# Performance work log

Hardware: AMD Instinct MI355X
Metric: run time of the kernel (lower is better)

The kernel has to match this reference:

```python
import jax, jax.numpy as jnp
import numpy as np

ALPHA = 0.2      # LeakyReLU negative slope
DROPOUT_P = 0.1  # torch F.dropout default training=True, so it IS applied
D_OUT = 128


def setup_inputs() -> dict:
    key = jax.random.key(0)
    k1, k2, k3 = jax.random.split(key, 3)
    N, D_IN = 8192, 128
    batch = jax.random.normal(k1, (N, D_IN), dtype=jnp.float32)
    # xavier_uniform gain=1.414 scale for faithfulness of magnitude
    w = jax.random.uniform(k2, (D_IN, D_OUT), dtype=jnp.float32, minval=-1.0, maxval=1.0) * (1.414 * np.sqrt(6.0 / (D_IN + D_OUT)))
    a = jax.random.uniform(k3, (2 * D_OUT, 1), dtype=jnp.float32, minval=-1.0, maxval=1.0) * (1.414 * np.sqrt(6.0 / (2 * D_OUT + 1)))
    return {"batch": batch, "w": w, "a": a}


def reference(batch, w, a):
    h = batch.reshape(-1, w.shape[0])            # [N, D_in]
    Wh = h @ w                                   # [N, D_out]
    Wh1 = Wh @ a[:D_OUT, :]                      # [N, 1]
    Wh2 = Wh @ a[D_OUT:, :]                      # [N, 1]
    e = Wh1 + Wh2.T                              # [N, N] additive scores
    e = jnp.where(e > 0, e, ALPHA * e)           # LeakyReLU
    attention = jax.nn.softmax(e, axis=1)        # row softmax
    # dropout with a fixed key (deterministic reference)
    keep = jax.random.bernoulli(jax.random.key(42), 1.0 - DROPOUT_P, attention.shape)
    attention = jnp.where(keep, attention / (1.0 - DROPOUT_P), 0.0)
    h_prime = attention @ Wh                     # [N, D_out]
    return jax.nn.elu(h_prime)                   # concat=True -> elu
```

## Files before the change

### kernel.cpp

```cpp
#include <hip/hip_runtime.h>
#include <stdint.h>

#define ALPHA 0.2f
#define LOG2E 1.4426950408889634f

typedef __bf16 bf16x8 __attribute__((ext_vector_type(8)));
typedef float f32x4 __attribute__((ext_vector_type(4)));

__device__ __forceinline__ uint32_t rotl32(uint32_t x, int r) {
  return __builtin_amdgcn_alignbit(x, x, 32 - r);
}

__device__ __forceinline__ uint32_t tf_mix(uint32_t f) {
  const uint32_t ks1 = 42u, ks2 = 0x1BD11BF0u;
  uint32_t x0 = 0u;
  uint32_t x1 = f + ks1;
#define TFR(r) { x0 += x1; x1 = rotl32(x1, r); x1 ^= x0; }
  TFR(13) TFR(15) TFR(26) TFR(6)  x0 += ks1; x1 += ks2 + 1u;
  TFR(17) TFR(29) TFR(16) TFR(24) x0 += ks2; x1 += 0u  + 2u;
  TFR(13) TFR(15) TFR(26) TFR(6)  x0 += 0u;  x1 += ks1 + 3u;
  TFR(17) TFR(29) TFR(16) TFR(24) x0 += ks1; x1 += ks2 + 4u;
  TFR(13) TFR(15) TFR(26) TFR(6)  x0 += ks2; x1 += 0u  + 5u;
#undef TFR
  return x0 ^ x1;
}

__device__ __forceinline__ void tf_mix4(uint32_t f0, uint32_t f1, uint32_t f2, uint32_t f3,
                                        uint32_t& o0, uint32_t& o1, uint32_t& o2, uint32_t& o3) {
  const uint32_t ks1 = 42u, ks2 = 0x1BD11BF0u;
  uint32_t a0 = 0u, a1 = 0u, a2 = 0u, a3 = 0u;
  uint32_t b0 = f0 + ks1, b1 = f1 + ks1, b2 = f2 + ks1, b3 = f3 + ks1;
#define Q4(rr)                                                              \
  a0 += b0; a1 += b1; a2 += b2; a3 += b3;                                   \
  b0 = rotl32(b0, rr); b1 = rotl32(b1, rr);                                 \
  b2 = rotl32(b2, rr); b3 = rotl32(b3, rr);                                 \
  b0 ^= a0; b1 ^= a1; b2 ^= a2; b3 ^= a3;
#define KADD(c0, c1)                                                        \
  a0 += (c0); a1 += (c0); a2 += (c0); a3 += (c0);                           \
  b0 += (c1); b1 += (c1); b2 += (c1); b3 += (c1);
  Q4(13) Q4(15) Q4(26) Q4(6)  KADD(ks1, ks2 + 1u)
  Q4(17) Q4(29) Q4(16) Q4(24) KADD(ks2, 0u + 2u)
  Q4(13) Q4(15) Q4(26) Q4(6)  KADD(0u, ks1 + 3u)
  Q4(17) Q4(29) Q4(16) Q4(24) KADD(ks1, ks2 + 4u)
  Q4(13) Q4(15) Q4(26) Q4(6)  KADD(ks2, 0u + 5u)
#undef Q4
#undef KADD
  o0 = a0 ^ b0; o1 = a1 ^ b1; o2 = a2 ^ b2; o3 = a3 ^ b3;
}

__device__ __forceinline__ unsigned short f2bf(float f) {
  uint32_t u = __float_as_uint(f);
  return (unsigned short)((u + 0x7fffu + ((u >> 16) & 1u)) >> 16);
}

__global__ __launch_bounds__(256) void wh_kernel(
    const float* __restrict__ batch, const float* __restrict__ w,
    const float* __restrict__ a, unsigned short* __restrict__ whb2,
    float* __restrict__ s1, float* __restrict__ s2, uint32_t* __restrict__ s2key) {
  __shared__ float whlds[32][128];
  int t = threadIdx.x;
  int i0 = blockIdx.x * 32;
  int d = t & 127, rg = t >> 7;
  int ib = i0 + rg * 16;
  float acc[16];
#pragma unroll
  for (int r = 0; r < 16; ++r) acc[r] = 0.f;
  for (int k = 0; k < 128; k += 4) {
    float wv0 = w[(k + 0) * 128 + d];
    float wv1 = w[(k + 1) * 128 + d];
    float wv2 = w[(k + 2) * 128 + d];
    float wv3 = w[(k + 3) * 128 + d];
#pragma unroll
    for (int r = 0; r < 16; ++r) {
      float4 b4 = *(const float4*)&batch[(ib + r) * 128 + k];
      acc[r] = fmaf(b4.w, wv3, fmaf(b4.z, wv2, fmaf(b4.y, wv1, fmaf(b4.x, wv0, acc[r]))));
    }
  }
  unsigned short hb[16];
#pragma unroll
  for (int r = 0; r < 16; ++r) {
    whlds[rg * 16 + r][d] = acc[r];
    hb[r] = f2bf(acc[r]);
  }
  uint32_t pk[8];
#pragma unroll
  for (int q = 0; q < 8; ++q) pk[q] = (uint32_t)hb[2 * q] | ((uint32_t)hb[2 * q + 1] << 16);
  uint32_t base0 = (((uint32_t)(ib >> 3) * 16u + (uint32_t)(d & 15)) * 8u + (uint32_t)(d >> 4)) * 8u;
  *(uint4*)&whb2[base0]        = make_uint4(pk[0], pk[1], pk[2], pk[3]);
  *(uint4*)&whb2[base0 + 1024] = make_uint4(pk[4], pk[5], pk[6], pk[7]);
  __syncthreads();
  int rr = t >> 3, seg = t & 7, c0 = seg * 16;
  const float* wr = &whlds[rr][c0];
  float p1 = 0.f, p2 = 0.f;
#pragma unroll
  for (int c = 0; c < 16; ++c) {
    float v = wr[c];
    p1 = fmaf(v, a[c0 + c], p1);
    p2 = fmaf(v, a[128 + c0 + c], p2);
  }
  p1 += __shfl_xor(p1, 1, 64); p1 += __shfl_xor(p1, 2, 64); p1 += __shfl_xor(p1, 4, 64);
  p2 += __shfl_xor(p2, 1, 64); p2 += __shfl_xor(p2, 2, 64); p2 += __shfl_xor(p2, 4, 64);
  if (seg == 0) { s1[i0 + rr] = p1; s2[i0 + rr] = p2; }
  float v = (seg == 0) ? p2 : -3.4e38f;
#pragma unroll
  for (int m = 1; m <= 32; m <<= 1) v = fmaxf(v, __shfl_xor(v, m, 64));
  if ((t & 63) == 0) {
    uint32_t b = __float_as_uint(v);
    uint32_t key = (b & 0x80000000u) ? ~b : (b | 0x80000000u);
    atomicMax(s2key, key);
  }
}

__global__ __launch_bounds__(256, 4) void gat_main(
    const float* __restrict__ s1, const float* __restrict__ s2g,
    const uint32_t* __restrict__ s2key, const unsigned short* __restrict__ whb2,
    float* __restrict__ pacc, float* __restrict__ pz) {
  __shared__ __align__(16) float smem[4160];
  int t = threadIdx.x;
  int rb = blockIdx.x >> 2, ck = blockIdx.x & 3;
  int R0 = rb * 16, C0 = ck * 2048;

  for (int k = t; k < 512; k += 256) {
    float4 v4 = ((const float4*)(s2g + C0))[k];
    float sL, e1, e2;
    sL = v4.x * LOG2E; e1 = __builtin_amdgcn_exp2f(sL); e2 = __builtin_amdgcn_exp2f(ALPHA * sL);
    ((float2*)smem)[k * 4 + 0] = make_float2(e1, e2);
    sL = v4.y * LOG2E; e1 = __builtin_amdgcn_exp2f(sL); e2 = __builtin_amdgcn_exp2f(ALPHA * sL);
    ((float2*)smem)[k * 4 + 1] = make_float2(e1, e2);
    sL = v4.z * LOG2E; e1 = __builtin_amdgcn_exp2f(sL); e2 = __builtin_amdgcn_exp2f(ALPHA * sL);
    ((float2*)smem)[k * 4 + 2] = make_float2(e1, e2);
    sL = v4.w * LOG2E; e1 = __builtin_amdgcn_exp2f(sL); e2 = __builtin_amdgcn_exp2f(ALPHA * sL);
    ((float2*)smem)[k * 4 + 3] = make_float2(e1, e2);
  }

  uint32_t kk = *s2key;
  uint32_t mb = (kk & 0x80000000u) ? (kk ^ 0x80000000u) : ~kk;
  float s2maxL = __uint_as_float(mb) * LOG2E;

  int w = t >> 6, lane = t & 63;
  int r = lane & 15, q = lane >> 4;

  float s1L = s1[R0 + r] * LOG2E;
  float xmL = s1L + s2maxL;
  float mrL = fmaxf(xmL, ALPHA * xmL);
  float F1 = __builtin_amdgcn_exp2f(s1L - mrL);
  float F2 = __builtin_amdgcn_exp2f(fmaf(ALPHA, s1L, -mrL));

  uint32_t fcur = (uint32_t)(R0 + r) * 8192u + (uint32_t)(C0 + w * 32 + q * 8);
  uint32_t voff = (((uint32_t)(C0 / 8 + w * 4 + q)) * 16u + (uint32_t)r) * 128u;
  const char* pB = (const char*)whb2;
  const float2* Eb = ((const float2*)smem) + w * 32 + q * 8;

  f32x4 acc0 = {0,0,0,0}, acc1 = {0,0,0,0}, acc2 = {0,0,0,0}, acc3 = {0,0,0,0};
  f32x4 acc4 = {0,0,0,0}, acc5 = {0,0,0,0}, acc6 = {0,0,0,0}, acc7 = {0,0,0,0};
  float z0 = 0.f, z1 = 0.f;
  const uint32_t KTH = 0xE6666600u;

  __syncthreads();

#pragma unroll 1
  for (int it = 0; it < 16; ++it) {
    bf16x8 B0 = *(const bf16x8*)(pB + voff);
    bf16x8 B1 = *(const bf16x8*)(pB + voff + 16);
    bf16x8 B2 = *(const bf16x8*)(pB + voff + 32);
    bf16x8 B3 = *(const bf16x8*)(pB + voff + 48);
    bf16x8 B4 = *(const bf16x8*)(pB + voff + 64);
    bf16x8 B5 = *(const bf16x8*)(pB + voff + 80);
    bf16x8 B6 = *(const bf16x8*)(pB + voff + 96);
    bf16x8 B7 = *(const bf16x8*)(pB + voff + 112);
    float4 E01 = *(const float4*)(Eb);
    float4 E23 = *(const float4*)(Eb + 2);
    float4 E45 = *(const float4*)(Eb + 4);
    float4 E67 = *(const float4*)(Eb + 6);
    __builtin_amdgcn_sched_barrier(0);

    bf16x8 A;
    {
      uint32_t h0, h1, h2, h3;
      tf_mix4(fcur + 0u, fcur + 1u, fcur + 2u, fcur + 3u, h0, h1, h2, h3);
      float pv0 = fmaxf(F1 * E01.x, F2 * E01.y);
      float pv1 = fmaxf(F1 * E01.z, F2 * E01.w);
      float pv2 = fmaxf(F1 * E23.x, F2 * E23.y);
      float pv3 = fmaxf(F1 * E23.z, F2 * E23.w);
      z0 += pv0 + pv1;
      z1 += pv2 + pv3;
      A[0] = (__bf16)((h0 < KTH) ? pv0 : 0.f);
      A[1] = (__bf16)((h1 < KTH) ? pv1 : 0.f);
      A[2] = (__bf16)((h2 < KTH) ? pv2 : 0.f);
      A[3] = (__bf16)((h3 < KTH) ? pv3 : 0.f);
    }
    {
      uint32_t h4, h5, h6, h7;
      tf_mix4(fcur + 4u, fcur + 5u, fcur + 6u, fcur + 7u, h4, h5, h6, h7);
      float pv4 = fmaxf(F1 * E45.x, F2 * E45.y);
      float pv5 = fmaxf(F1 * E45.z, F2 * E45.w);
      float pv6 = fmaxf(F1 * E67.x, F2 * E67.y);
      float pv7 = fmaxf(F1 * E67.z, F2 * E67.w);
      z0 += pv4 + pv5;
      z1 += pv6 + pv7;
      A[4] = (__bf16)((h4 < KTH) ? pv4 : 0.f);
      A[5] = (__bf16)((h5 < KTH) ? pv5 : 0.f);
      A[6] = (__bf16)((h6 < KTH) ? pv6 : 0.f);
      A[7] = (__bf16)((h7 < KTH) ? pv7 : 0.f);
    }

    acc0 = __builtin_amdgcn_mfma_f32_16x16x32_bf16(A, B0, acc0, 0, 0, 0);
    acc1 = __builtin_amdgcn_mfma_f32_16x16x32_bf16(A, B1, acc1, 0, 0, 0);
    acc2 = __builtin_amdgcn_mfma_f32_16x16x32_bf16(A, B2, acc2, 0, 0, 0);
    acc3 = __builtin_amdgcn_mfma_f32_16x16x32_bf16(A, B3, acc3, 0, 0, 0);
    acc4 = __builtin_amdgcn_mfma_f32_16x16x32_bf16(A, B4, acc4, 0, 0, 0);
    acc5 = __builtin_amdgcn_mfma_f32_16x16x32_bf16(A, B5, acc5, 0, 0, 0);
    acc6 = __builtin_amdgcn_mfma_f32_16x16x32_bf16(A, B6, acc6, 0, 0, 0);
    acc7 = __builtin_amdgcn_mfma_f32_16x16x32_bf16(A, B7, acc7, 0, 0, 0);

    fcur += 128u;
    voff += 32768u;
    Eb += 128;
  }
  float z = z0 + z1;

  __syncthreads();
  float zq = z + __shfl_xor(z, 16, 64);
  zq += __shfl_xor(zq, 32, 64);
  if (lane < 16) smem[4096 + w * 16 + lane] = zq;

  float* red = smem;
  int wbase = w * 1024 + q * 256 + r;
#define STOREG(u, accN)                                \
  {                                                    \
    red[wbase + 0 * 64 + (u) * 16] = accN[0];          \
    red[wbase + 1 * 64 + (u) * 16] = accN[1];          \
    red[wbase + 2 * 64 + (u) * 16] = accN[2];          \
    red[wbase + 3 * 64 + (u) * 16] = accN[3];          \
  }
  STOREG(0, acc0) STOREG(1, acc1) STOREG(2, acc2) STOREG(3, acc3)
  __syncthreads();
#pragma unroll
  for (int k2 = 0; k2 < 4; ++k2) {
    int idx = t * 4 + k2;
    float s = (red[idx] + red[1024 + idx]) + (red[2048 + idx] + red[3072 + idx]);
    atomicAdd(&pacc[(R0 + (idx >> 6)) * 128 + (idx & 63)], s);
  }
  __syncthreads();
  STOREG(0, acc4) STOREG(1, acc5) STOREG(2, acc6) STOREG(3, acc7)
#undef STOREG
  __syncthreads();
#pragma unroll
  for (int k2 = 0; k2 < 4; ++k2) {
    int idx = t * 4 + k2;
    float s = (red[idx] + red[1024 + idx]) + (red[2048 + idx] + red[3072 + idx]);
    atomicAdd(&pacc[(R0 + (idx >> 6)) * 128 + 64 + (idx & 63)], s);
  }
  if (t < 16) {
    float zs = (smem[4096 + t] + smem[4112 + t]) + (smem[4128 + t] + smem[4144 + t]);
    atomicAdd(&pz[R0 + t], zs);
  }
}

__global__ __launch_bounds__(256) void gat_final(
    const float* __restrict__ pacc, const float* __restrict__ pz,
    float* __restrict__ out) {
  int t = threadIdx.x;
  int row = blockIdx.x * 8 + (t >> 5);
  int d4 = (t & 31) * 4;
  float zinv = 1.f / (0.9f * pz[row]);
  float4 p = *(const float4*)&pacc[row * 128 + d4];
  float4 o;
  float v;
  v = p.x * zinv; o.x = v > 0.f ? v : expm1f(v);
  v = p.y * zinv; o.y = v > 0.f ? v : expm1f(v);
  v = p.z * zinv; o.z = v > 0.f ? v : expm1f(v);
  v = p.w * zinv; o.w = v > 0.f ? v : expm1f(v);
  *(float4*)&out[row * 128 + d4] = o;
}

extern "C" void kernel_launch(void* const* d_in, const int* in_sizes, int n_in,
                              void* d_out, int out_size, void* d_ws, size_t ws_size,
                              hipStream_t stream) {
  const float* batch = (const float*)d_in[0];
  const float* w = (const float*)d_in[1];
  const float* a = (const float*)d_in[2];
  float* out = (float*)d_out;
  char* ws = (char*)d_ws;
  float* pacc = (float*)ws;
  float* pz = (float*)(ws + 4194304);
  uint32_t* s2key = (uint32_t*)(ws + 4194304 + 32768);
  unsigned short* whb2 = (unsigned short*)(ws + 4194304 + 32768 + 64);
  float* s1 = (float*)(ws + 4194304 + 32768 + 64 + 2097152);
  float* s2 = (float*)(ws + 4194304 + 32768 + 64 + 2097152 + 32768);

  hipMemsetAsync(ws, 0, 4194304 + 32768 + 64, stream);
  wh_kernel<<<256, 256, 0, stream>>>(batch, w, a, whb2, s1, s2, s2key);
  gat_main<<<2048, 256, 0, stream>>>(s1, s2, s2key, whb2, pacc, pz);
  gat_final<<<1024, 256, 0, stream>>>(pacc, pz, out);
}
```

Measured before the change: 176.5 us.

## Compute exp per element in-loop, split columns in two, and replace atomics with slabs

The main kernel no longer precomputes two exponentials per column in shared memory. It stores log2-scaled s2 and evaluates exp2 of the LeakyReLU score per element, which halves the LDS reads per iteration. Each block now covers 4096 columns instead of 2048, so there are half as many blocks. Each block writes its partial accumulators and row sums to a per-split slab instead of using global atomics, and the final kernel adds the two slabs. The large workspace memset shrinks to the 64-byte key. The trade is more transcendental work per element and fewer blocks with a longer loop. The B loads are also split into two halves around the first half of the compute.

Measured after the change: 211.1 us. 19.6% more time.

```diff
diff --git a/kernel.cpp b/kernel.cpp
--- a/kernel.cpp
+++ b/kernel.cpp
@@ -9,20 +9,6 @@
 
 __device__ __forceinline__ uint32_t rotl32(uint32_t x, int r) {
   return __builtin_amdgcn_alignbit(x, x, 32 - r);
-}
-
-__device__ __forceinline__ uint32_t tf_mix(uint32_t f) {
-  const uint32_t ks1 = 42u, ks2 = 0x1BD11BF0u;
-  uint32_t x0 = 0u;
-  uint32_t x1 = f + ks1;
-#define TFR(r) { x0 += x1; x1 = rotl32(x1, r); x1 ^= x0; }
-  TFR(13) TFR(15) TFR(26) TFR(6)  x0 += ks1; x1 += ks2 + 1u;
-  TFR(17) TFR(29) TFR(16) TFR(24) x0 += ks2; x1 += 0u  + 2u;
-  TFR(13) TFR(15) TFR(26) TFR(6)  x0 += 0u;  x1 += ks1 + 3u;
-  TFR(17) TFR(29) TFR(16) TFR(24) x0 += ks1; x1 += ks2 + 4u;
-  TFR(13) TFR(15) TFR(26) TFR(6)  x0 += ks2; x1 += 0u  + 5u;
-#undef TFR
-  return x0 ^ x1;
 }
 
 __device__ __forceinline__ void tf_mix4(uint32_t f0, uint32_t f1, uint32_t f2, uint32_t f3,
@@ -114,23 +100,18 @@
 __global__ __launch_bounds__(256, 4) void gat_main(
     const float* __restrict__ s1, const float* __restrict__ s2g,
     const uint32_t* __restrict__ s2key, const unsigned short* __restrict__ whb2,
-    float* __restrict__ pacc, float* __restrict__ pz) {
+    float* __restrict__ pslab, float* __restrict__ zslab) {
   __shared__ __align__(16) float smem[4160];
   int t = threadIdx.x;
-  int rb = blockIdx.x >> 2, ck = blockIdx.x & 3;
-  int R0 = rb * 16, C0 = ck * 2048;
-
-  for (int k = t; k < 512; k += 256) {
+  int rb = blockIdx.x >> 1, ck = blockIdx.x & 1;
+  int R0 = rb * 16, C0 = ck * 4096;
+  float* ps = pslab + ck * (8192 * 128);
+  float* zs = zslab + ck * 8192;
+
+  for (int k = t; k < 1024; k += 256) {
     float4 v4 = ((const float4*)(s2g + C0))[k];
-    float sL, e1, e2;
-    sL = v4.x * LOG2E; e1 = __builtin_amdgcn_exp2f(sL); e2 = __builtin_amdgcn_exp2f(ALPHA * sL);
-    ((float2*)smem)[k * 4 + 0] = make_float2(e1, e2);
-    sL = v4.y * LOG2E; e1 = __builtin_amdgcn_exp2f(sL); e2 = __builtin_amdgcn_exp2f(ALPHA * sL);
-    ((float2*)smem)[k * 4 + 1] = make_float2(e1, e2);
-    sL = v4.z * LOG2E; e1 = __builtin_amdgcn_exp2f(sL); e2 = __builtin_amdgcn_exp2f(ALPHA * sL);
-    ((float2*)smem)[k * 4 + 2] = make_float2(e1, e2);
-    sL = v4.w * LOG2E; e1 = __builtin_amdgcn_exp2f(sL); e2 = __builtin_amdgcn_exp2f(ALPHA * sL);
-    ((float2*)smem)[k * 4 + 3] = make_float2(e1, e2);
+    v4.x *= LOG2E; v4.y *= LOG2E; v4.z *= LOG2E; v4.w *= LOG2E;
+    ((float4*)smem)[k] = v4;
   }
 
   uint32_t kk = *s2key;
@@ -143,61 +124,60 @@
   float s1L = s1[R0 + r] * LOG2E;
   float xmL = s1L + s2maxL;
   float mrL = fmaxf(xmL, ALPHA * xmL);
-  float F1 = __builtin_amdgcn_exp2f(s1L - mrL);
-  float F2 = __builtin_amdgcn_exp2f(fmaf(ALPHA, s1L, -mrL));
+  float Ar = s1L - mrL;
+  float Cr = fmaf(ALPHA, s1L, -mrL);
 
   uint32_t fcur = (uint32_t)(R0 + r) * 8192u + (uint32_t)(C0 + w * 32 + q * 8);
   uint32_t voff = (((uint32_t)(C0 / 8 + w * 4 + q)) * 16u + (uint32_t)r) * 128u;
   const char* pB = (const char*)whb2;
-  const float2* Eb = ((const float2*)smem) + w * 32 + q * 8;
+  const float* sjb = smem + w * 32 + q * 8;
 
   f32x4 acc0 = {0,0,0,0}, acc1 = {0,0,0,0}, acc2 = {0,0,0,0}, acc3 = {0,0,0,0};
   f32x4 acc4 = {0,0,0,0}, acc5 = {0,0,0,0}, acc6 = {0,0,0,0}, acc7 = {0,0,0,0};
-  float z0 = 0.f, z1 = 0.f;
+  float z0a = 0.f, z1a = 0.f;
   const uint32_t KTH = 0xE6666600u;
 
   __syncthreads();
 
 #pragma unroll 1
-  for (int it = 0; it < 16; ++it) {
+  for (int it = 0; it < 32; ++it) {
     bf16x8 B0 = *(const bf16x8*)(pB + voff);
     bf16x8 B1 = *(const bf16x8*)(pB + voff + 16);
     bf16x8 B2 = *(const bf16x8*)(pB + voff + 32);
     bf16x8 B3 = *(const bf16x8*)(pB + voff + 48);
-    bf16x8 B4 = *(const bf16x8*)(pB + voff + 64);
-    bf16x8 B5 = *(const bf16x8*)(pB + voff + 80);
-    bf16x8 B6 = *(const bf16x8*)(pB + voff + 96);
-    bf16x8 B7 = *(const bf16x8*)(pB + voff + 112);
-    float4 E01 = *(const float4*)(Eb);
-    float4 E23 = *(const float4*)(Eb + 2);
-    float4 E45 = *(const float4*)(Eb + 4);
-    float4 E67 = *(const float4*)(Eb + 6);
+    float4 sj0 = *(const float4*)(sjb + it * 128);
+    float4 sj1 = *(const float4*)(sjb + it * 128 + 4);
     __builtin_amdgcn_sched_barrier(0);
 
     bf16x8 A;
     {
       uint32_t h0, h1, h2, h3;
       tf_mix4(fcur + 0u, fcur + 1u, fcur + 2u, fcur + 3u, h0, h1, h2, h3);
-      float pv0 = fmaxf(F1 * E01.x, F2 * E01.y);
-      float pv1 = fmaxf(F1 * E01.z, F2 * E01.w);
-      float pv2 = fmaxf(F1 * E23.x, F2 * E23.y);
-      float pv3 = fmaxf(F1 * E23.z, F2 * E23.w);
-      z0 += pv0 + pv1;
-      z1 += pv2 + pv3;
+      float pv0 = __builtin_amdgcn_exp2f(fmaxf(Ar + sj0.x, fmaf(ALPHA, sj0.x, Cr)));
+      float pv1 = __builtin_amdgcn_exp2f(fmaxf(Ar + sj0.y, fmaf(ALPHA, sj0.y, Cr)));
+      float pv2 = __builtin_amdgcn_exp2f(fmaxf(Ar + sj0.z, fmaf(ALPHA, sj0.z, Cr)));
+      float pv3 = __builtin_amdgcn_exp2f(fmaxf(Ar + sj0.w, fmaf(ALPHA, sj0.w, Cr)));
+      z0a += pv0 + pv1;
+      z1a += pv2 + pv3;
       A[0] = (__bf16)((h0 < KTH) ? pv0 : 0.f);
       A[1] = (__bf16)((h1 < KTH) ? pv1 : 0.f);
       A[2] = (__bf16)((h2 < KTH) ? pv2 : 0.f);
       A[3] = (__bf16)((h3 < KTH) ? pv3 : 0.f);
     }
+    bf16x8 B4 = *(const bf16x8*)(pB + voff + 64);
+    bf16x8 B5 = *(const bf16x8*)(pB + voff + 80);
+    bf16x8 B6 = *(const bf16x8*)(pB + voff + 96);
+    bf16x8 B7 = *(const bf16x8*)(pB + voff + 112);
+    __builtin_amdgcn_sched_barrier(0);
     {
       uint32_t h4, h5, h6, h7;
       tf_mix4(fcur + 4u, fcur + 5u, fcur + 6u, fcur + 7u, h4, h5, h6, h7);
-      float pv4 = fmaxf(F1 * E45.x, F2 * E45.y);
-      float pv5 = fmaxf(F1 * E45.z, F2 * E45.w);
-      float pv6 = fmaxf(F1 * E67.x, F2 * E67.y);
-      float pv7 = fmaxf(F1 * E67.z, F2 * E67.w);
-      z0 += pv4 + pv5;
-      z1 += pv6 + pv7;
+      float pv4 = __builtin_amdgcn_exp2f(fmaxf(Ar + sj1.x, fmaf(ALPHA, sj1.x, Cr)));
+      float pv5 = __builtin_amdgcn_exp2f(fmaxf(Ar + sj1.y, fmaf(ALPHA, sj1.y, Cr)));
+      float pv6 = __builtin_amdgcn_exp2f(fmaxf(Ar + sj1.z, fmaf(ALPHA, sj1.z, Cr)));
+      float pv7 = __builtin_amdgcn_exp2f(fmaxf(Ar + sj1.w, fmaf(ALPHA, sj1.w, Cr)));
+      z0a += pv4 + pv5;
+      z1a += pv6 + pv7;
       A[4] = (__bf16)((h4 < KTH) ? pv4 : 0.f);
       A[5] = (__bf16)((h5 < KTH) ? pv5 : 0.f);
       A[6] = (__bf16)((h6 < KTH) ? pv6 : 0.f);
@@ -215,9 +195,8 @@
 
     fcur += 128u;
     voff += 32768u;
-    Eb += 128;
-  }
-  float z = z0 + z1;
+  }
+  float z = z0a + z1a;
 
   __syncthreads();
   float zq = z + __shfl_xor(z, 16, 64);
@@ -239,7 +218,7 @@
   for (int k2 = 0; k2 < 4; ++k2) {
     int idx = t * 4 + k2;
     float s = (red[idx] + red[1024 + idx]) + (red[2048 + idx] + red[3072 + idx]);
-    atomicAdd(&pacc[(R0 + (idx >> 6)) * 128 + (idx & 63)], s);
+    ps[(R0 + (idx >> 6)) * 128 + (idx & 63)] = s;
   }
   __syncthreads();
   STOREG(0, acc4) STOREG(1, acc5) STOREG(2, acc6) STOREG(3, acc7)
@@ -249,28 +228,29 @@
   for (int k2 = 0; k2 < 4; ++k2) {
     int idx = t * 4 + k2;
     float s = (red[idx] + red[1024 + idx]) + (red[2048 + idx] + red[3072 + idx]);
-    atomicAdd(&pacc[(R0 + (idx >> 6)) * 128 + 64 + (idx & 63)], s);
+    ps[(R0 + (idx >> 6)) * 128 + 64 + (idx & 63)] = s;
   }
   if (t < 16) {
-    float zs = (smem[4096 + t] + smem[4112 + t]) + (smem[4128 + t] + smem[4144 + t]);
-    atomicAdd(&pz[R0 + t], zs);
+    float zsum = (smem[4096 + t] + smem[4112 + t]) + (smem[4128 + t] + smem[4144 + t]);
+    zs[R0 + t] = zsum;
   }
 }
 
 __global__ __launch_bounds__(256) void gat_final(
-    const float* __restrict__ pacc, const float* __restrict__ pz,
+    const float* __restrict__ pslab, const float* __restrict__ zslab,
     float* __restrict__ out) {
   int t = threadIdx.x;
   int row = blockIdx.x * 8 + (t >> 5);
   int d4 = (t & 31) * 4;
-  float zinv = 1.f / (0.9f * pz[row]);
-  float4 p = *(const float4*)&pacc[row * 128 + d4];
+  float zinv = 1.f / (0.9f * (zslab[row] + zslab[8192 + row]));
+  float4 p0 = *(const float4*)&pslab[row * 128 + d4];
+  float4 p1 = *(const float4*)&pslab[8192 * 128 + row * 128 + d4];
   float4 o;
   float v;
-  v = p.x * zinv; o.x = v > 0.f ? v : expm1f(v);
-  v = p.y * zinv; o.y = v > 0.f ? v : expm1f(v);
-  v = p.z * zinv; o.z = v > 0.f ? v : expm1f(v);
-  v = p.w * zinv; o.w = v > 0.f ? v : expm1f(v);
+  v = (p0.x + p1.x) * zinv; o.x = v > 0.f ? v : expm1f(v);
+  v = (p0.y + p1.y) * zinv; o.y = v > 0.f ? v : expm1f(v);
+  v = (p0.z + p1.z) * zinv; o.z = v > 0.f ? v : expm1f(v);
+  v = (p0.w + p1.w) * zinv; o.w = v > 0.f ? v : expm1f(v);
   *(float4*)&out[row * 128 + d4] = o;
 }
 
@@ -282,15 +262,15 @@
   const float* a = (const float*)d_in[2];
   float* out = (float*)d_out;
   char* ws = (char*)d_ws;
-  float* pacc = (float*)ws;
-  float* pz = (float*)(ws + 4194304);
-  uint32_t* s2key = (uint32_t*)(ws + 4194304 + 32768);
-  unsigned short* whb2 = (unsigned short*)(ws + 4194304 + 32768 + 64);
-  float* s1 = (float*)(ws + 4194304 + 32768 + 64 + 2097152);
-  float* s2 = (float*)(ws + 4194304 + 32768 + 64 + 2097152 + 32768);
-
-  hipMemsetAsync(ws, 0, 4194304 + 32768 + 64, stream);
+  float* pslab = (float*)ws;
+  float* zslab = (float*)(ws + 8388608);
+  uint32_t* s2key = (uint32_t*)(ws + 8388608 + 65536);
+  unsigned short* whb2 = (unsigned short*)(ws + 8388608 + 65536 + 64);
+  float* s1 = (float*)(ws + 8388608 + 65536 + 64 + 2097152);
+  float* s2 = (float*)(ws + 8388608 + 65536 + 64 + 2097152 + 32768);
+
+  (void)hipMemsetAsync(s2key, 0, 64, stream);
   wh_kernel<<<256, 256, 0, stream>>>(batch, w, a, whb2, s1, s2, s2key);
-  gat_main<<<2048, 256, 0, stream>>>(s1, s2, s2key, whb2, pacc, pz);
-  gat_final<<<1024, 256, 0, stream>>>(pacc, pz, out);
-}
+  gat_main<<<1024, 256, 0, stream>>>(s1, s2, s2key, whb2, pslab, zslab);
+  gat_final<<<1024, 256, 0, stream>>>(pslab, zslab, out);
+}
```
